# Kernel optimization log

Hardware: AMD Instinct MI355X
Metric: run time of the kernel (lower is better)

Reference implementation:

```python
import jax, jax.numpy as jnp
import numpy as np
from jax import lax

D_MODEL = 1024
D_STATE = 16
D_CONV = 4
D_INNER = 2048  # d_model * expand
B = 1
L = 1024


def setup_inputs() -> dict:
    key = jax.random.key(0)
    ks = jax.random.split(key, 8)
    nrm = lambda k, shape, s: jax.random.normal(k, shape, jnp.float32) * s
    x = nrm(ks[0], (B, L, D_MODEL), 1.0)
    in_proj_w = nrm(ks[1], (2 * D_INNER, D_MODEL), D_MODEL ** -0.5)
    conv_w = nrm(ks[2], (D_INNER, 1, D_CONV), D_CONV ** -0.5)
    conv_b = nrm(ks[3], (D_INNER,), 0.02)
    x_proj_w = nrm(ks[4], (D_INNER + 4 * D_STATE, D_INNER), D_INNER ** -0.5)
    # small dt so the log-cumsum-exp scan stays finite in fp32 over L steps
    dt_proj_w = nrm(ks[5], (D_INNER, D_INNER), 0.01 * D_INNER ** -0.5)
    dt_proj_b = jnp.full((D_INNER,), -6.0, jnp.float32)
    # faithful A_log init: real = -0.5*log(n), imag = pi*n
    n = np.arange(1, D_STATE + 1, dtype=np.float32)
    A_log_re = jnp.asarray(np.tile(np.log(n) * -0.5, (D_INNER, 1)))
    A_log_im = jnp.asarray(np.tile(np.pi * n, (D_INNER, 1)))
    D = jnp.ones((D_INNER,), jnp.float32)
    out_proj_w = nrm(ks[6], (D_MODEL, D_INNER), D_INNER ** -0.5)
    return dict(x=x, in_proj_w=in_proj_w, conv_w=conv_w, conv_b=conv_b,
                x_proj_w=x_proj_w, dt_proj_w=dt_proj_w, dt_proj_b=dt_proj_b,
                A_log_re=A_log_re, A_log_im=A_log_im, D=D, out_proj_w=out_proj_w)


def reference(x, in_proj_w, conv_w, conv_b, x_proj_w, dt_proj_w, dt_proj_b,
              A_log_re, A_log_im, D, out_proj_w):
    # input projection and gate split
    xz = x @ in_proj_w.T                          # (B, L, 2*d_inner)
    xc, z = jnp.split(xz, 2, axis=-1)
    # causal depthwise conv1d (torch pads both sides then truncates -> left pad only)
    xt = jnp.transpose(xc, (0, 2, 1))             # (B, d_inner, L)
    xp = jnp.pad(xt, ((0, 0), (0, 0), (D_CONV - 1, 0)))
    conv = lax.conv_general_dilated(
        xp, conv_w, window_strides=(1,), padding='VALID',
        dimension_numbers=('NCH', 'OIH', 'NCH'),
        feature_group_count=D_INNER) + conv_b[None, :, None]
    u = jnp.transpose(jax.nn.silu(conv), (0, 2, 1))  # (B, L, d_inner)
    # ssm parameter projection
    ssm = u @ x_proj_w.T                          # (B, L, d_inner + 4*d_state)
    delta = ssm[..., :D_INNER]
    B_re = ssm[..., D_INNER:D_INNER + D_STATE]
    B_im = ssm[..., D_INNER + D_STATE:D_INNER + 2 * D_STATE]
    C_re = ssm[..., D_INNER + 2 * D_STATE:D_INNER + 3 * D_STATE]
    C_im = ssm[..., D_INNER + 3 * D_STATE:]
    delta = jax.nn.softplus(delta @ dt_proj_w.T + dt_proj_b)  # (B, L, d_inner)
    Bc = (B_re + 1j * B_im).astype(jnp.complex64)             # (B, L, d_state)
    Cc = (C_re + 1j * C_im).astype(jnp.complex64)
    # complex selective scan via bilinear (Cayley) discretization + log-cumsum-exp
    A = -jnp.exp((A_log_re + 1j * A_log_im).astype(jnp.complex64))  # (d_inner, d_state)
    dt_c = delta[..., None].astype(jnp.complex64)             # (B, L, d_inner, 1)
    denom = 2.0 - dt_c * A                                    # (B, L, d_inner, d_state)
    numer = 2.0 + dt_c * A
    log_A_bar = jnp.log(numer) - jnp.log(denom)
    u_bar = (2.0 * dt_c / denom) * Bc[:, :, None, :] * u[..., None].astype(jnp.complex64)
    lc = jnp.cumsum(log_A_bar, axis=1)                        # cumulative log transition
    H = jnp.cumsum(jnp.exp(-lc) * u_bar, axis=1) * jnp.exp(lc)
    y = jnp.sum(Cc[:, :, None, :] * H, axis=-1).real + D * u  # (B, L, d_inner)
    y = y * jax.nn.silu(z)
    return y @ out_proj_w.T                                   # (B, L, d_model)
```

## Files before the change

### kernel.cpp

```cpp
#include <hip/hip_runtime.h>
#include <hip/hip_bf16.h>
#include <math.h>

#define L_SEQ   1024
#define DMODEL  1024
#define DINNER  2048
#define DSTATE  16
#define DCONV   4
#define NPROJ   (DINNER + 4 * DSTATE)
#define NCHUNK  16
#define CHUNK   64
#define NDN     (DINNER * DSTATE)

typedef __attribute__((ext_vector_type(8))) short  short8;
typedef __attribute__((ext_vector_type(4))) float  f32x4;
typedef __attribute__((ext_vector_type(4))) unsigned short us4;

__device__ __forceinline__ float softplus_f(float v) {
    return fmaxf(v, 0.f) + log1pf(expf(-fabsf(v)));
}
__device__ __forceinline__ float silu_f(float v) {
    return v * __builtin_amdgcn_rcpf(1.f + expf(-v));
}

__device__ __forceinline__ void split4(float4 v, us4& h, us4& l) {
    float vv[4] = {v.x, v.y, v.z, v.w};
    #pragma unroll
    for (int i = 0; i < 4; ++i) {
        unsigned b  = __float_as_uint(vv[i]);
        unsigned hb = b & 0xffff0000u;
        float    r  = vv[i] - __uint_as_float(hb);
        unsigned rb = __float_as_uint(r) + 0x8000u;
        h[i] = (unsigned short)(hb >> 16);
        l[i] = (unsigned short)(rb >> 16);
    }
}

template<int BM>
__global__ __launch_bounds__(256) void gemm_mfma_sk(
    const float* __restrict__ A, const float* __restrict__ W,
    float* __restrict__ Cp, int M, int N, int K, int lda)
{
    constexpr int MF = BM / 32;
    constexpr int NF = 2;
    __shared__ unsigned short sAh[BM * 40], sAl[BM * 40];
    __shared__ unsigned short sBh[64 * 40], sBl[64 * 40];

    const int tid  = threadIdx.x;
    const int w    = tid >> 6;
    const int lane = tid & 63;
    const int wr   = w >> 1;
    const int wc   = w & 1;
    const int lrow = lane & 15;
    const int lkb  = lane >> 4;
    const int row0 = blockIdx.y * BM;
    const int col0 = blockIdx.x * 64;

    const int KS   = K / gridDim.z;
    const int kbeg = blockIdx.z * KS;
    const int kend = kbeg + KS;

    const int srow = tid >> 3;
    const int sfq  = tid & 7;

    f32x4 acc[MF][NF];
    #pragma unroll
    for (int m = 0; m < MF; ++m)
        #pragma unroll
        for (int n = 0; n < NF; ++n)
            acc[m][n] = (f32x4){0.f, 0.f, 0.f, 0.f};

    for (int k0 = kbeg; k0 < kend; k0 += 32) {
        #pragma unroll
        for (int p = 0; p < BM / 32; ++p) {
            int r = srow + p * 32;
            float4 v = *reinterpret_cast<const float4*>(
                A + (size_t)(row0 + r) * lda + k0 + sfq * 4);
            us4 h, l;
            split4(v, h, l);
            *reinterpret_cast<us4*>(sAh + r * 40 + sfq * 4) = h;
            *reinterpret_cast<us4*>(sAl + r * 40 + sfq * 4) = l;
        }
        #pragma unroll
        for (int p = 0; p < 2; ++p) {
            int r = srow + p * 32;
            float4 v = *reinterpret_cast<const float4*>(
                W + (size_t)(col0 + r) * K + k0 + sfq * 4);
            us4 h, l;
            split4(v, h, l);
            *reinterpret_cast<us4*>(sBh + r * 40 + sfq * 4) = h;
            *reinterpret_cast<us4*>(sBl + r * 40 + sfq * 4) = l;
        }
        __syncthreads();

        short8 ah[MF], al[MF], bh[NF], bl[NF];
        #pragma unroll
        for (int m = 0; m < MF; ++m) {
            int off = (wr * (BM / 2) + m * 16 + lrow) * 40 + lkb * 8;
            ah[m] = *reinterpret_cast<const short8*>(sAh + off);
            al[m] = *reinterpret_cast<const short8*>(sAl + off);
        }
        #pragma unroll
        for (int n = 0; n < NF; ++n) {
            int off = (wc * 32 + n * 16 + lrow) * 40 + lkb * 8;
            bh[n] = *reinterpret_cast<const short8*>(sBh + off);
            bl[n] = *reinterpret_cast<const short8*>(sBl + off);
        }

        #pragma unroll
        for (int m = 0; m < MF; ++m)
            #pragma unroll
            for (int n = 0; n < NF; ++n) {
                acc[m][n] = __builtin_amdgcn_mfma_f32_16x16x32_bf16(
                    ah[m], bh[n], acc[m][n], 0, 0, 0);
                acc[m][n] = __builtin_amdgcn_mfma_f32_16x16x32_bf16(
                    ah[m], bl[n], acc[m][n], 0, 0, 0);
                acc[m][n] = __builtin_amdgcn_mfma_f32_16x16x32_bf16(
                    al[m], bh[n], acc[m][n], 0, 0, 0);
            }
        __syncthreads();
    }

    float* Cb = Cp + (size_t)blockIdx.z * M * N;
    #pragma unroll
    for (int m = 0; m < MF; ++m)
        #pragma unroll
        for (int n = 0; n < NF; ++n) {
            int gr0 = row0 + wr * (BM / 2) + m * 16 + lkb * 4;
            int gc  = col0 + wc * 32 + n * 16 + lrow;
            #pragma unroll
            for (int r = 0; r < 4; ++r)
                Cb[(size_t)(gr0 + r) * N + gc] = acc[m][n][r];
        }
}

template<int EPI>
__global__ __launch_bounds__(256) void reduce_splitk(
    const float* __restrict__ part, float* __restrict__ out,
    const float* __restrict__ bias, int size, int N, int nsplit)
{
    int i = (blockIdx.x * 256 + threadIdx.x) * 4;
    if (i >= size) return;
    float4 s = *reinterpret_cast<const float4*>(part + i);
    for (int p = 1; p < nsplit; ++p) {
        float4 v = *reinterpret_cast<const float4*>(part + (size_t)p * size + i);
        s.x += v.x; s.y += v.y; s.z += v.z; s.w += v.w;
    }
    if (EPI == 1) {
        int col = i % N;
        float4 b = *reinterpret_cast<const float4*>(bias + col);
        s.x = softplus_f(s.x + b.x); s.y = softplus_f(s.y + b.y);
        s.z = softplus_f(s.z + b.z); s.w = softplus_f(s.w + b.w);
    }
    *reinterpret_cast<float4*>(out + i) = s;
}

__global__ __launch_bounds__(256) void conv_silu_kernel(
    const float* __restrict__ xz, const float* __restrict__ cw,
    const float* __restrict__ cb, float* __restrict__ u)
{
    int idx = blockIdx.x * 256 + threadIdx.x;
    int l = idx >> 11;
    int d = idx & (DINNER - 1);
    float acc = cb[d];
    #pragma unroll
    for (int k = 0; k < DCONV; ++k) {
        int ls = l - (DCONV - 1) + k;
        float xv = (ls >= 0) ? xz[(size_t)ls * (2 * DINNER) + d] : 0.f;
        acc = fmaf(xv, cw[d * DCONV + k], acc);
    }
    u[idx] = silu_f(acc);
}

__device__ __forceinline__ void bilinear_coef(
    float dt, float a_re, float a_im,
    float& ab_re, float& ab_im, float& co_re, float& co_im)
{
    float dre = fmaf(-dt, a_re, 2.f);
    float dim = -dt * a_im;
    float inv = __builtin_amdgcn_rcpf(fmaf(dre, dre, dim * dim));
    float qre = dre * inv;
    float qim = -dim * inv;
    ab_re = fmaf(4.f, qre, -1.f);
    ab_im = 4.f * qim;
    float t2 = dt + dt;
    co_re = t2 * qre;
    co_im = t2 * qim;
}

__global__ __launch_bounds__(64) void scan_chunk_kernel(
    const float* __restrict__ delta, const float* __restrict__ ssm,
    const float* __restrict__ u,
    const float* __restrict__ A_log_re, const float* __restrict__ A_log_im,
    float2* __restrict__ Pc, float2* __restrict__ Sc)
{
    const int b = blockIdx.x;
    const int chunk = b >> 9;
    const int d4 = b & 511;
    const int tid = threadIdx.x;
    const int n = tid & 15;
    const int dloc = tid >> 4;
    const int d = d4 * 4 + dloc;

    const float mag  = expf(A_log_re[d * DSTATE + n]);
    const float alim = A_log_im[d * DSTATE + n];
    const float a_re = -mag * cosf(alim);
    const float a_im = -mag * sinf(alim);

    float p_re = 1.f, p_im = 0.f;
    float s_re = 0.f, s_im = 0.f;

    const int l0 = chunk * CHUNK;
    #pragma unroll 4
    for (int i = 0; i < CHUNK; ++i) {
        const int l = l0 + i;
        float dt = delta[(size_t)l * DINNER + d];
        float uv = u[(size_t)l * DINNER + d];
        const float* srow = ssm + (size_t)l * NPROJ + DINNER;
        float br = srow[n];
        float bi = srow[DSTATE + n];

        float ab_re, ab_im, co_re, co_im;
        bilinear_coef(dt, a_re, a_im, ab_re, ab_im, co_re, co_im);
        float cbr = co_re * br - co_im * bi;
        float cbi = co_re * bi + co_im * br;
        float ub_re = cbr * uv;
        float ub_im = cbi * uv;

        float sr = ab_re * s_re - ab_im * s_im + ub_re;
        float si = ab_re * s_im + ab_im * s_re + ub_im;
        s_re = sr; s_im = si;
        float pr = ab_re * p_re - ab_im * p_im;
        float pi = ab_re * p_im + ab_im * p_re;
        p_re = pr; p_im = pi;
    }

    const int idx = chunk * NDN + d * DSTATE + n;
    Pc[idx] = make_float2(p_re, p_im);
    Sc[idx] = make_float2(s_re, s_im);
}

__global__ __launch_bounds__(256) void scan_combine_kernel(
    float2* __restrict__ Pc, const float2* __restrict__ Sc)
{
    const int td = blockIdx.x * 256 + threadIdx.x;
    float h_re = 0.f, h_im = 0.f;
    #pragma unroll
    for (int c = 0; c < NCHUNK; ++c) {
        float2 p = Pc[c * NDN + td];
        float2 s = Sc[c * NDN + td];
        Pc[c * NDN + td] = make_float2(h_re, h_im);
        float nr = s.x + p.x * h_re - p.y * h_im;
        float ni = s.y + p.x * h_im + p.y * h_re;
        h_re = nr; h_im = ni;
    }
}

__global__ __launch_bounds__(64) void scan_final_kernel(
    const float* __restrict__ delta, const float* __restrict__ ssm,
    const float* __restrict__ u, const float* __restrict__ xz,
    const float* __restrict__ A_log_re, const float* __restrict__ A_log_im,
    const float* __restrict__ Dvec, const float2* __restrict__ Hin,
    float* __restrict__ y)
{
    const int b = blockIdx.x;
    const int chunk = b >> 9;
    const int d4 = b & 511;
    const int tid = threadIdx.x;
    const int n = tid & 15;
    const int dloc = tid >> 4;
    const int d = d4 * 4 + dloc;

    const float mag  = expf(A_log_re[d * DSTATE + n]);
    const float alim = A_log_im[d * DSTATE + n];
    const float a_re = -mag * cosf(alim);
    const float a_im = -mag * sinf(alim);
    const float Dd   = Dvec[d];

    float2 h0 = Hin[chunk * NDN + d * DSTATE + n];
    float h_re = h0.x, h_im = h0.y;

    const int l0 = chunk * CHUNK;
    #pragma unroll 2
    for (int i = 0; i < CHUNK; ++i) {
        const int l = l0 + i;
        float dt = delta[(size_t)l * DINNER + d];
        float uv = u[(size_t)l * DINNER + d];
        const float* srow = ssm + (size_t)l * NPROJ + DINNER;
        float br = srow[n];
        float bi = srow[DSTATE + n];
        float cr = srow[2 * DSTATE + n];
        float ci = srow[3 * DSTATE + n];

        float ab_re, ab_im, co_re, co_im;
        bilinear_coef(dt, a_re, a_im, ab_re, ab_im, co_re, co_im);
        float cbr = co_re * br - co_im * bi;
        float cbi = co_re * bi + co_im * br;
        float ub_re = cbr * uv;
        float ub_im = cbi * uv;

        float hr = ab_re * h_re - ab_im * h_im + ub_re;
        float hi = ab_re * h_im + ab_im * h_re + ub_im;
        h_re = hr; h_im = hi;

        float contrib = cr * h_re - ci * h_im;
        contrib += __shfl_xor(contrib, 1, 16);
        contrib += __shfl_xor(contrib, 2, 16);
        contrib += __shfl_xor(contrib, 4, 16);
        contrib += __shfl_xor(contrib, 8, 16);
        if (n == 0) {
            float zv = xz[(size_t)l * (2 * DINNER) + DINNER + d];
            float yv = contrib + Dd * uv;
            y[(size_t)l * DINNER + d] = yv * silu_f(zv);
        }
    }
}

extern "C" void kernel_launch(void* const* d_in, const int* in_sizes, int n_in,
                              void* d_out, int out_size, void* d_ws, size_t ws_size,
                              hipStream_t stream)
{
    const float* x         = (const float*)d_in[0];
    const float* in_proj_w = (const float*)d_in[1];
    const float* conv_w    = (const float*)d_in[2];
    const float* conv_b    = (const float*)d_in[3];
    const float* x_proj_w  = (const float*)d_in[4];
    const float* dt_proj_w = (const float*)d_in[5];
    const float* dt_proj_b = (const float*)d_in[6];
    const float* A_log_re  = (const float*)d_in[7];
    const float* A_log_im  = (const float*)d_in[8];
    const float* Dvec      = (const float*)d_in[9];
    const float* out_proj_w= (const float*)d_in[10];
    float* out = (float*)d_out;

    float* ws    = (float*)d_ws;
    float* xz    = ws;
    float* u     = xz    + (size_t)L_SEQ * 2 * DINNER;
    float* ssm   = u     + (size_t)L_SEQ * DINNER;
    float* delta = ssm   + (size_t)L_SEQ * NPROJ;
    float* y     = delta + (size_t)L_SEQ * DINNER;
    float2* Pc   = (float2*)(y + (size_t)L_SEQ * DINNER);
    float2* Sc   = Pc + (size_t)NCHUNK * NDN;
    float* part  = (float*)(Sc + (size_t)NCHUNK * NDN);

    gemm_mfma_sk<128><<<dim3((2 * DINNER) / 64, L_SEQ / 128, 2), 256, 0, stream>>>(
        x, in_proj_w, part, L_SEQ, 2 * DINNER, DMODEL, DMODEL);
    reduce_splitk<0><<<(L_SEQ * 2 * DINNER) / 1024, 256, 0, stream>>>(
        part, xz, nullptr, L_SEQ * 2 * DINNER, 2 * DINNER, 2);

    conv_silu_kernel<<<(L_SEQ * DINNER) / 256, 256, 0, stream>>>(xz, conv_w, conv_b, u);

    gemm_mfma_sk<128><<<dim3(NPROJ / 64, L_SEQ / 128, 4), 256, 0, stream>>>(
        u, x_proj_w, part, L_SEQ, NPROJ, DINNER, DINNER);
    reduce_splitk<0><<<(L_SEQ * NPROJ) / 1024, 256, 0, stream>>>(
        part, ssm, nullptr, L_SEQ * NPROJ, NPROJ, 4);

    gemm_mfma_sk<128><<<dim3(DINNER / 64, L_SEQ / 128, 4), 256, 0, stream>>>(
        ssm, dt_proj_w, part, L_SEQ, DINNER, DINNER, NPROJ);
    reduce_splitk<1><<<(L_SEQ * DINNER) / 1024, 256, 0, stream>>>(
        part, delta, dt_proj_b, L_SEQ * DINNER, DINNER, 4);

    scan_chunk_kernel<<<(DINNER / 4) * NCHUNK, 64, 0, stream>>>(
        delta, ssm, u, A_log_re, A_log_im, Pc, Sc);
    scan_combine_kernel<<<NDN / 256, 256, 0, stream>>>(Pc, Sc);
    scan_final_kernel<<<(DINNER / 4) * NCHUNK, 64, 0, stream>>>(
        delta, ssm, u, xz, A_log_re, A_log_im, Dvec, Pc, y);

    gemm_mfma_sk<64><<<dim3(DMODEL / 64, L_SEQ / 64, 4), 256, 0, stream>>>(
        y, out_proj_w, part, L_SEQ, DMODEL, DINNER, DINNER);
    reduce_splitk<0><<<(L_SEQ * DMODEL) / 1024, 256, 0, stream>>>(
        part, out, nullptr, L_SEQ * DMODEL, DMODEL, 4);
}
```

Baseline: 420.3 us.

## Pre-split GEMM activations into bf16 hi/lo in producers; scan two channels per thread

Producer kernels (conv, split-k reduce, scan final) now write bf16 hi/lo halves of their fp32 outputs, so three GEMMs load ready-made bf16 A tiles instead of splitting fp32 inside every tile load. This removes repeated split work, since each A element was otherwise re-split once per column block. The scan kernels also process two d channels per thread, halving the block count and sharing the B/C loads between the two channels. The cost is extra global writes and workspace for the hi/lo buffers, and more registers per scan thread.

```diff
diff --git a/kernel.cpp b/kernel.cpp
--- a/kernel.cpp
+++ b/kernel.cpp
@@ -13,6 +13,7 @@
 #define NDN     (DINNER * DSTATE)
 
 typedef __attribute__((ext_vector_type(8))) short  short8;
+typedef __attribute__((ext_vector_type(8))) unsigned short us8;
 typedef __attribute__((ext_vector_type(4))) float  f32x4;
 typedef __attribute__((ext_vector_type(4))) unsigned short us4;
 
@@ -23,6 +24,14 @@
     return v * __builtin_amdgcn_rcpf(1.f + expf(-v));
 }
 
+__device__ __forceinline__ void split1(float x, unsigned short& h, unsigned short& l) {
+    unsigned b  = __float_as_uint(x);
+    unsigned hb = b & 0xffff0000u;
+    float    r  = x - __uint_as_float(hb);
+    unsigned rb = __float_as_uint(r) + 0x8000u;
+    h = (unsigned short)(hb >> 16);
+    l = (unsigned short)(rb >> 16);
+}
 __device__ __forceinline__ void split4(float4 v, us4& h, us4& l) {
     float vv[4] = {v.x, v.y, v.z, v.w};
     #pragma unroll
@@ -134,10 +143,112 @@
         }
 }
 
-template<int EPI>
+template<int BM>
+__global__ __launch_bounds__(256) void gemm_bf16a_sk(
+    const unsigned short* __restrict__ Ah, const unsigned short* __restrict__ Al,
+    const float* __restrict__ W, float* __restrict__ Cp, int M, int N, int K)
+{
+    constexpr int MF = BM / 32;
+    constexpr int NF = 2;
+    constexpr int NL = BM / 64;
+    __shared__ unsigned short sAh[BM * 40], sAl[BM * 40];
+    __shared__ unsigned short sBh[64 * 40], sBl[64 * 40];
+
+    const int tid  = threadIdx.x;
+    const int w    = tid >> 6;
+    const int lane = tid & 63;
+    const int wr   = w >> 1;
+    const int wc   = w & 1;
+    const int lrow = lane & 15;
+    const int lkb  = lane >> 4;
+    const int row0 = blockIdx.y * BM;
+    const int col0 = blockIdx.x * 64;
+
+    const int KS   = K / gridDim.z;
+    const int kbeg = blockIdx.z * KS;
+    const int kend = kbeg + KS;
+
+    const int srow = tid >> 3;
+    const int sfq  = tid & 7;
+
+    f32x4 acc[MF][NF];
+    #pragma unroll
+    for (int m = 0; m < MF; ++m)
+        #pragma unroll
+        for (int n = 0; n < NF; ++n)
+            acc[m][n] = (f32x4){0.f, 0.f, 0.f, 0.f};
+
+    for (int k0 = kbeg; k0 < kend; k0 += 32) {
+        #pragma unroll
+        for (int j = 0; j < NL; ++j) {
+            int idx8 = j * 256 + tid;
+            int r    = idx8 >> 2;
+            int kq   = (idx8 & 3) * 8;
+            size_t g = (size_t)(row0 + r) * K + k0 + kq;
+            *reinterpret_cast<us8*>(sAh + r * 40 + kq) =
+                *reinterpret_cast<const us8*>(Ah + g);
+            *reinterpret_cast<us8*>(sAl + r * 40 + kq) =
+                *reinterpret_cast<const us8*>(Al + g);
+        }
+        #pragma unroll
+        for (int p = 0; p < 2; ++p) {
+            int r = srow + p * 32;
+            float4 v = *reinterpret_cast<const float4*>(
+                W + (size_t)(col0 + r) * K + k0 + sfq * 4);
+            us4 h, l;
+            split4(v, h, l);
+            *reinterpret_cast<us4*>(sBh + r * 40 + sfq * 4) = h;
+            *reinterpret_cast<us4*>(sBl + r * 40 + sfq * 4) = l;
+        }
+        __syncthreads();
+
+        short8 ah[MF], al[MF], bh[NF], bl[NF];
+        #pragma unroll
+        for (int m = 0; m < MF; ++m) {
+            int off = (wr * (BM / 2) + m * 16 + lrow) * 40 + lkb * 8;
+            ah[m] = *reinterpret_cast<const short8*>(sAh + off);
+            al[m] = *reinterpret_cast<const short8*>(sAl + off);
+        }
+        #pragma unroll
+        for (int n = 0; n < NF; ++n) {
+            int off = (wc * 32 + n * 16 + lrow) * 40 + lkb * 8;
+            bh[n] = *reinterpret_cast<const short8*>(sBh + off);
+            bl[n] = *reinterpret_cast<const short8*>(sBl + off);
+        }
+
+        #pragma unroll
+        for (int m = 0; m < MF; ++m)
+            #pragma unroll
+            for (int n = 0; n < NF; ++n) {
+                acc[m][n] = __builtin_amdgcn_mfma_f32_16x16x32_bf16(
+                    ah[m], bh[n], acc[m][n], 0, 0, 0);
+                acc[m][n] = __builtin_amdgcn_mfma_f32_16x16x32_bf16(
+                    ah[m], bl[n], acc[m][n], 0, 0, 0);
+                acc[m][n] = __builtin_amdgcn_mfma_f32_16x16x32_bf16(
+                    al[m], bh[n], acc[m][n], 0, 0, 0);
+            }
+        __syncthreads();
+    }
+
+    float* Cb = Cp + (size_t)blockIdx.z * M * N;
+    #pragma unroll
+    for (int m = 0; m < MF; ++m)
+        #pragma unroll
+        for (int n = 0; n < NF; ++n) {
+            int gr0 = row0 + wr * (BM / 2) + m * 16 + lkb * 4;
+            int gc  = col0 + wc * 32 + n * 16 + lrow;
+            #pragma unroll
+            for (int r = 0; r < 4; ++r)
+                Cb[(size_t)(gr0 + r) * N + gc] = acc[m][n][r];
+        }
+}
+
+template<int EPI, int SPLIT>
 __global__ __launch_bounds__(256) void reduce_splitk(
     const float* __restrict__ part, float* __restrict__ out,
-    const float* __restrict__ bias, int size, int N, int nsplit)
+    const float* __restrict__ bias,
+    unsigned short* __restrict__ oh, unsigned short* __restrict__ ol,
+    int size, int N, int nsplit)
 {
     int i = (blockIdx.x * 256 + threadIdx.x) * 4;
     if (i >= size) return;
@@ -153,11 +264,22 @@
         s.z = softplus_f(s.z + b.z); s.w = softplus_f(s.w + b.w);
     }
     *reinterpret_cast<float4*>(out + i) = s;
+    if (SPLIT == 1) {
+        int col = i % N;
+        if (col < 2048) {
+            int row = i / N;
+            us4 h, l;
+            split4(s, h, l);
+            *reinterpret_cast<us4*>(oh + (size_t)row * 2048 + col) = h;
+            *reinterpret_cast<us4*>(ol + (size_t)row * 2048 + col) = l;
+        }
+    }
 }
 
 __global__ __launch_bounds__(256) void conv_silu_kernel(
     const float* __restrict__ xz, const float* __restrict__ cw,
-    const float* __restrict__ cb, float* __restrict__ u)
+    const float* __restrict__ cb, float* __restrict__ u,
+    unsigned short* __restrict__ uh, unsigned short* __restrict__ ul)
 {
     int idx = blockIdx.x * 256 + threadIdx.x;
     int l = idx >> 11;
@@ -169,7 +291,11 @@
         float xv = (ls >= 0) ? xz[(size_t)ls * (2 * DINNER) + d] : 0.f;
         acc = fmaf(xv, cw[d * DCONV + k], acc);
     }
-    u[idx] = silu_f(acc);
+    float v = silu_f(acc);
+    u[idx] = v;
+    unsigned short h, lo;
+    split1(v, h, lo);
+    uh[idx] = h; ul[idx] = lo;
 }
 
 __device__ __forceinline__ void bilinear_coef(
@@ -195,49 +321,69 @@
     float2* __restrict__ Pc, float2* __restrict__ Sc)
 {
     const int b = blockIdx.x;
-    const int chunk = b >> 9;
-    const int d4 = b & 511;
+    const int chunk = b >> 8;
+    const int dg = b & 255;
     const int tid = threadIdx.x;
     const int n = tid & 15;
     const int dloc = tid >> 4;
-    const int d = d4 * 4 + dloc;
-
-    const float mag  = expf(A_log_re[d * DSTATE + n]);
-    const float alim = A_log_im[d * DSTATE + n];
-    const float a_re = -mag * cosf(alim);
-    const float a_im = -mag * sinf(alim);
-
-    float p_re = 1.f, p_im = 0.f;
-    float s_re = 0.f, s_im = 0.f;
+    const int d0 = dg * 8 + dloc;
+    const int d1 = d0 + 4;
+
+    float m0 = expf(A_log_re[d0 * DSTATE + n]);
+    float i0 = A_log_im[d0 * DSTATE + n];
+    float a0r = -m0 * cosf(i0), a0i = -m0 * sinf(i0);
+    float m1 = expf(A_log_re[d1 * DSTATE + n]);
+    float i1 = A_log_im[d1 * DSTATE + n];
+    float a1r = -m1 * cosf(i1), a1i = -m1 * sinf(i1);
+
+    float p0r = 1.f, p0i = 0.f, s0r = 0.f, s0i = 0.f;
+    float p1r = 1.f, p1i = 0.f, s1r = 0.f, s1i = 0.f;
 
     const int l0 = chunk * CHUNK;
-    #pragma unroll 4
+    #pragma unroll 2
     for (int i = 0; i < CHUNK; ++i) {
         const int l = l0 + i;
-        float dt = delta[(size_t)l * DINNER + d];
-        float uv = u[(size_t)l * DINNER + d];
+        float dt0 = delta[(size_t)l * DINNER + d0];
+        float dt1 = delta[(size_t)l * DINNER + d1];
+        float uv0 = u[(size_t)l * DINNER + d0];
+        float uv1 = u[(size_t)l * DINNER + d1];
         const float* srow = ssm + (size_t)l * NPROJ + DINNER;
         float br = srow[n];
         float bi = srow[DSTATE + n];
 
-        float ab_re, ab_im, co_re, co_im;
-        bilinear_coef(dt, a_re, a_im, ab_re, ab_im, co_re, co_im);
-        float cbr = co_re * br - co_im * bi;
-        float cbi = co_re * bi + co_im * br;
-        float ub_re = cbr * uv;
-        float ub_im = cbi * uv;
-
-        float sr = ab_re * s_re - ab_im * s_im + ub_re;
-        float si = ab_re * s_im + ab_im * s_re + ub_im;
-        s_re = sr; s_im = si;
-        float pr = ab_re * p_re - ab_im * p_im;
-        float pi = ab_re * p_im + ab_im * p_re;
-        p_re = pr; p_im = pi;
-    }
-
-    const int idx = chunk * NDN + d * DSTATE + n;
-    Pc[idx] = make_float2(p_re, p_im);
-    Sc[idx] = make_float2(s_re, s_im);
+        float abr, abi, cor, coi;
+        bilinear_coef(dt0, a0r, a0i, abr, abi, cor, coi);
+        {
+            float cbr = cor * br - coi * bi;
+            float cbi = cor * bi + coi * br;
+            float ur = cbr * uv0, ui = cbi * uv0;
+            float sr = abr * s0r - abi * s0i + ur;
+            float si = abr * s0i + abi * s0r + ui;
+            s0r = sr; s0i = si;
+            float pr = abr * p0r - abi * p0i;
+            float pi = abr * p0i + abi * p0r;
+            p0r = pr; p0i = pi;
+        }
+        bilinear_coef(dt1, a1r, a1i, abr, abi, cor, coi);
+        {
+            float cbr = cor * br - coi * bi;
+            float cbi = cor * bi + coi * br;
+            float ur = cbr * uv1, ui = cbi * uv1;
+            float sr = abr * s1r - abi * s1i + ur;
+            float si = abr * s1i + abi * s1r + ui;
+            s1r = sr; s1i = si;
+            float pr = abr * p1r - abi * p1i;
+            float pi = abr * p1i + abi * p1r;
+            p1r = pr; p1i = pi;
+        }
+    }
+
+    int idx0 = chunk * NDN + d0 * DSTATE + n;
+    int idx1 = chunk * NDN + d1 * DSTATE + n;
+    Pc[idx0] = make_float2(p0r, p0i);
+    Sc[idx0] = make_float2(s0r, s0i);
+    Pc[idx1] = make_float2(p1r, p1i);
+    Sc[idx1] = make_float2(s1r, s1i);
 }
 
 __global__ __launch_bounds__(256) void scan_combine_kernel(
@@ -261,57 +407,82 @@
     const float* __restrict__ u, const float* __restrict__ xz,
     const float* __restrict__ A_log_re, const float* __restrict__ A_log_im,
     const float* __restrict__ Dvec, const float2* __restrict__ Hin,
-    float* __restrict__ y)
+    unsigned short* __restrict__ yh, unsigned short* __restrict__ yl)
 {
     const int b = blockIdx.x;
-    const int chunk = b >> 9;
-    const int d4 = b & 511;
+    const int chunk = b >> 8;
+    const int dg = b & 255;
     const int tid = threadIdx.x;
     const int n = tid & 15;
     const int dloc = tid >> 4;
-    const int d = d4 * 4 + dloc;
-
-    const float mag  = expf(A_log_re[d * DSTATE + n]);
-    const float alim = A_log_im[d * DSTATE + n];
-    const float a_re = -mag * cosf(alim);
-    const float a_im = -mag * sinf(alim);
-    const float Dd   = Dvec[d];
-
-    float2 h0 = Hin[chunk * NDN + d * DSTATE + n];
-    float h_re = h0.x, h_im = h0.y;
+    const int d0 = dg * 8 + dloc;
+    const int d1 = d0 + 4;
+
+    float m0 = expf(A_log_re[d0 * DSTATE + n]);
+    float i0 = A_log_im[d0 * DSTATE + n];
+    float a0r = -m0 * cosf(i0), a0i = -m0 * sinf(i0);
+    float m1 = expf(A_log_re[d1 * DSTATE + n]);
+    float i1 = A_log_im[d1 * DSTATE + n];
+    float a1r = -m1 * cosf(i1), a1i = -m1 * sinf(i1);
+    float Dd0 = Dvec[d0], Dd1 = Dvec[d1];
+
+    float2 h0 = Hin[chunk * NDN + d0 * DSTATE + n];
+    float2 h1 = Hin[chunk * NDN + d1 * DSTATE + n];
+    float h0r = h0.x, h0i = h0.y, h1r = h1.x, h1i = h1.y;
 
     const int l0 = chunk * CHUNK;
     #pragma unroll 2
     for (int i = 0; i < CHUNK; ++i) {
         const int l = l0 + i;
-        float dt = delta[(size_t)l * DINNER + d];
-        float uv = u[(size_t)l * DINNER + d];
+        float dt0 = delta[(size_t)l * DINNER + d0];
+        float dt1 = delta[(size_t)l * DINNER + d1];
+        float uv0 = u[(size_t)l * DINNER + d0];
+        float uv1 = u[(size_t)l * DINNER + d1];
         const float* srow = ssm + (size_t)l * NPROJ + DINNER;
         float br = srow[n];
         float bi = srow[DSTATE + n];
         float cr = srow[2 * DSTATE + n];
         float ci = srow[3 * DSTATE + n];
 
-        float ab_re, ab_im, co_re, co_im;
-        bilinear_coef(dt, a_re, a_im, ab_re, ab_im, co_re, co_im);
-        float cbr = co_re * br - co_im * bi;
-        float cbi = co_re * bi + co_im * br;
-        float ub_re = cbr * uv;
-        float ub_im = cbi * uv;
-
-        float hr = ab_re * h_re - ab_im * h_im + ub_re;
-        float hi = ab_re * h_im + ab_im * h_re + ub_im;
-        h_re = hr; h_im = hi;
-
-        float contrib = cr * h_re - ci * h_im;
-        contrib += __shfl_xor(contrib, 1, 16);
-        contrib += __shfl_xor(contrib, 2, 16);
-        contrib += __shfl_xor(contrib, 4, 16);
-        contrib += __shfl_xor(contrib, 8, 16);
+        float abr, abi, cor, coi;
+        bilinear_coef(dt0, a0r, a0i, abr, abi, cor, coi);
+        float c0;
+        {
+            float cbr = cor * br - coi * bi;
+            float cbi = cor * bi + coi * br;
+            float hr = abr * h0r - abi * h0i + cbr * uv0;
+            float hi = abr * h0i + abi * h0r + cbi * uv0;
+            h0r = hr; h0i = hi;
+            c0 = cr * h0r - ci * h0i;
+        }
+        bilinear_coef(dt1, a1r, a1i, abr, abi, cor, coi);
+        float c1;
+        {
+            float cbr = cor * br - coi * bi;
+            float cbi = cor * bi + coi * br;
+            float hr = abr * h1r - abi * h1i + cbr * uv1;
+            float hi = abr * h1i + abi * h1r + cbi * uv1;
+            h1r = hr; h1i = hi;
+            c1 = cr * h1r - ci * h1i;
+        }
+        c0 += __shfl_xor(c0, 1, 16);
+        c0 += __shfl_xor(c0, 2, 16);
+        c0 += __shfl_xor(c0, 4, 16);
+        c0 += __shfl_xor(c0, 8, 16);
+        c1 += __shfl_xor(c1, 1, 16);
+        c1 += __shfl_xor(c1, 2, 16);
+        c1 += __shfl_xor(c1, 4, 16);
+        c1 += __shfl_xor(c1, 8, 16);
         if (n == 0) {
-            float zv = xz[(size_t)l * (2 * DINNER) + DINNER + d];
-            float yv = contrib + Dd * uv;
-            y[(size_t)l * DINNER + d] = yv * silu_f(zv);
+            float zv0 = xz[(size_t)l * (2 * DINNER) + DINNER + d0];
+            float zv1 = xz[(size_t)l * (2 * DINNER) + DINNER + d1];
+            float o0 = (c0 + Dd0 * uv0) * silu_f(zv0);
+            float o1 = (c1 + Dd1 * uv1) * silu_f(zv1);
+            unsigned short hh, ll;
+            split1(o0, hh, ll);
+            yh[(size_t)l * DINNER + d0] = hh; yl[(size_t)l * DINNER + d0] = ll;
+            split1(o1, hh, ll);
+            yh[(size_t)l * DINNER + d1] = hh; yl[(size_t)l * DINNER + d1] = ll;
         }
     }
 }
@@ -338,36 +509,42 @@
     float* u     = xz    + (size_t)L_SEQ * 2 * DINNER;
     float* ssm   = u     + (size_t)L_SEQ * DINNER;
     float* delta = ssm   + (size_t)L_SEQ * NPROJ;
-    float* y     = delta + (size_t)L_SEQ * DINNER;
-    float2* Pc   = (float2*)(y + (size_t)L_SEQ * DINNER);
+    float2* Pc   = (float2*)(delta + (size_t)L_SEQ * DINNER);
     float2* Sc   = Pc + (size_t)NCHUNK * NDN;
     float* part  = (float*)(Sc + (size_t)NCHUNK * NDN);
+    unsigned short* uh = (unsigned short*)(part + (size_t)4 * L_SEQ * NPROJ);
+    unsigned short* ul = uh + (size_t)L_SEQ * DINNER;
+    unsigned short* sh = ul + (size_t)L_SEQ * DINNER;
+    unsigned short* sl = sh + (size_t)L_SEQ * DINNER;
+    unsigned short* yh = sl + (size_t)L_SEQ * DINNER;
+    unsigned short* yl = yh + (size_t)L_SEQ * DINNER;
 
     gemm_mfma_sk<128><<<dim3((2 * DINNER) / 64, L_SEQ / 128, 2), 256, 0, stream>>>(
         x, in_proj_w, part, L_SEQ, 2 * DINNER, DMODEL, DMODEL);
-    reduce_splitk<0><<<(L_SEQ * 2 * DINNER) / 1024, 256, 0, stream>>>(
-        part, xz, nullptr, L_SEQ * 2 * DINNER, 2 * DINNER, 2);
-
-    conv_silu_kernel<<<(L_SEQ * DINNER) / 256, 256, 0, stream>>>(xz, conv_w, conv_b, u);
-
-    gemm_mfma_sk<128><<<dim3(NPROJ / 64, L_SEQ / 128, 4), 256, 0, stream>>>(
-        u, x_proj_w, part, L_SEQ, NPROJ, DINNER, DINNER);
-    reduce_splitk<0><<<(L_SEQ * NPROJ) / 1024, 256, 0, stream>>>(
-        part, ssm, nullptr, L_SEQ * NPROJ, NPROJ, 4);
-
-    gemm_mfma_sk<128><<<dim3(DINNER / 64, L_SEQ / 128, 4), 256, 0, stream>>>(
-        ssm, dt_proj_w, part, L_SEQ, DINNER, DINNER, NPROJ);
-    reduce_splitk<1><<<(L_SEQ * DINNER) / 1024, 256, 0, stream>>>(
-        part, delta, dt_proj_b, L_SEQ * DINNER, DINNER, 4);
-
-    scan_chunk_kernel<<<(DINNER / 4) * NCHUNK, 64, 0, stream>>>(
+    reduce_splitk<0, 0><<<(L_SEQ * 2 * DINNER) / 1024, 256, 0, stream>>>(
+        part, xz, nullptr, nullptr, nullptr, L_SEQ * 2 * DINNER, 2 * DINNER, 2);
+
+    conv_silu_kernel<<<(L_SEQ * DINNER) / 256, 256, 0, stream>>>(
+        xz, conv_w, conv_b, u, uh, ul);
+
+    gemm_bf16a_sk<128><<<dim3(NPROJ / 64, L_SEQ / 128, 4), 256, 0, stream>>>(
+        uh, ul, x_proj_w, part, L_SEQ, NPROJ, DINNER);
+    reduce_splitk<0, 1><<<(L_SEQ * NPROJ) / 1024, 256, 0, stream>>>(
+        part, ssm, nullptr, sh, sl, L_SEQ * NPROJ, NPROJ, 4);
+
+    gemm_bf16a_sk<128><<<dim3(DINNER / 64, L_SEQ / 128, 4), 256, 0, stream>>>(
+        sh, sl, dt_proj_w, part, L_SEQ, DINNER, DINNER);
+    reduce_splitk<1, 0><<<(L_SEQ * DINNER) / 1024, 256, 0, stream>>>(
+        part, delta, dt_proj_b, nullptr, nullptr, L_SEQ * DINNER, DINNER, 4);
+
+    scan_chunk_kernel<<<(DINNER / 8) * NCHUNK, 64, 0, stream>>>(
         delta, ssm, u, A_log_re, A_log_im, Pc, Sc);
     scan_combine_kernel<<<NDN / 256, 256, 0, stream>>>(Pc, Sc);
-    scan_final_kernel<<<(DINNER / 4) * NCHUNK, 64, 0, stream>>>(
-        delta, ssm, u, xz, A_log_re, A_log_im, Dvec, Pc, y);
-
-    gemm_mfma_sk<64><<<dim3(DMODEL / 64, L_SEQ / 64, 4), 256, 0, stream>>>(
-        y, out_proj_w, part, L_SEQ, DMODEL, DINNER, DINNER);
-    reduce_splitk<0><<<(L_SEQ * DMODEL) / 1024, 256, 0, stream>>>(
-        part, out, nullptr, L_SEQ * DMODEL, DMODEL, 4);
-}
+    scan_final_kernel<<<(DINNER / 8) * NCHUNK, 64, 0, stream>>>(
+        delta, ssm, u, xz, A_log_re, A_log_im, Dvec, Pc, yh, yl);
+
+    gemm_bf16a_sk<64><<<dim3(DMODEL / 64, L_SEQ / 64, 4), 256, 0, stream>>>(
+        yh, yl, out_proj_w, part, L_SEQ, DMODEL, DINNER);
+    reduce_splitk<0, 0><<<(L_SEQ * DMODEL) / 1024, 256, 0, stream>>>(
+        part, out, nullptr, nullptr, nullptr, L_SEQ * DMODEL, DMODEL, 4);
+}
```

After: 438.6 us. +4.4%, slower.
